# Optimization experiments

Measured on AMD Instinct MI355X. Metric: run time of the kernel, lower is better.

The kernel has to match this reference:

```python
import jax, jax.numpy as jnp
import numpy as np

N_HEAD = 16
D_MODEL = 1024
HEAD_DIM = D_MODEL // N_HEAD
B, S = 2, 2048


def setup_inputs() -> dict:
    key = jax.random.key(0)
    ks = jax.random.split(key, 7)
    qry = jax.random.normal(ks[0], (B, S, D_MODEL), dtype=jnp.float32)
    k_in = jax.random.normal(ks[1], (B, S, D_MODEL), dtype=jnp.float32)
    v_in = jax.random.normal(ks[2], (B, S, D_MODEL), dtype=jnp.float32)
    # causal boolean mask (B, S_q, S_k) as asserted in SelfAttention.forward
    attn_mask = jnp.broadcast_to(jnp.tril(jnp.ones((S, S), dtype=bool)), (B, S, S))
    scale = 1.0 / np.sqrt(D_MODEL)
    Wq = jax.random.normal(ks[3], (D_MODEL, D_MODEL), dtype=jnp.float32) * scale
    Wk = jax.random.normal(ks[4], (D_MODEL, D_MODEL), dtype=jnp.float32) * scale
    Wv = jax.random.normal(ks[5], (D_MODEL, D_MODEL), dtype=jnp.float32) * scale
    Wo = jax.random.normal(ks[6], (D_MODEL, D_MODEL), dtype=jnp.float32) * scale
    return {"qry": qry, "key": k_in, "val": v_in, "attn_mask": attn_mask,
            "Wq": Wq, "Wk": Wk, "Wv": Wv, "Wo": Wo}


def reference(qry, key, val, attn_mask, Wq, Wk, Wv, Wo):
    Bq, Sq, _ = qry.shape
    # torch Linear: y = x @ W.T (no bias)
    q = (qry @ Wq.T).reshape(Bq, Sq, N_HEAD, HEAD_DIM).transpose(0, 2, 1, 3)
    k = (key @ Wk.T).reshape(Bq, -1, N_HEAD, HEAD_DIM).transpose(0, 2, 1, 3)
    v = (val @ Wv.T).reshape(Bq, -1, N_HEAD, HEAD_DIM).transpose(0, 2, 1, 3)
    # scores: [B, H, Sq, Sk]
    scores = jnp.einsum('bhqd,bhkd->bhqk', q, k) / jnp.sqrt(jnp.float32(HEAD_DIM * N_HEAD) / N_HEAD)
    # attn_bias: 0 where mask True, -inf where False; broadcast over heads
    bias = jnp.where(attn_mask[:, None, :, :], 0.0, -jnp.inf).astype(scores.dtype)
    attn_weights = jax.nn.softmax(scores + bias, axis=-1)
    attn_feats = jnp.einsum('bhqk,bhkd->bhqd', attn_weights, v)
    attn_feats = attn_feats.transpose(0, 2, 1, 3).reshape(Bq, Sq, D_MODEL)
    output = attn_feats @ Wo.T
    return output, attn_weights
```

## Files before the change

kernel.cpp:

```cpp
#include <hip/hip_runtime.h>
#include <hip/hip_bf16.h>
#include <cstdint>
#include <cstddef>

#define DM 1024
#define NH 16
#define HD 64
#define BB 2
#define SS 2048

typedef __attribute__((ext_vector_type(4))) float f32x4;
typedef __attribute__((ext_vector_type(8))) short bf16x8;

typedef __attribute__((address_space(1))) const void GV;
typedef __attribute__((address_space(3))) void LV;

__global__ __launch_bounds__(256) void cvt_all(
    const float* s0, const float* s1, const float* s2, const float* s3,
    const float* s4, const float* s5, const float* s6,
    __hip_bfloat16* d0, __hip_bfloat16* d1, __hip_bfloat16* d2, __hip_bfloat16* d3,
    __hip_bfloat16* d4, __hip_bfloat16* d5, __hip_bfloat16* d6) {
    const float* s; __hip_bfloat16* d; int n4;
    switch (blockIdx.y) {
        case 0: s = s0; d = d0; n4 = 1 << 20; break;
        case 1: s = s1; d = d1; n4 = 1 << 20; break;
        case 2: s = s2; d = d2; n4 = 1 << 20; break;
        case 3: s = s3; d = d3; n4 = 1 << 18; break;
        case 4: s = s4; d = d4; n4 = 1 << 18; break;
        case 5: s = s5; d = d5; n4 = 1 << 18; break;
        default: s = s6; d = d6; n4 = 1 << 18; break;
    }
    for (int i = blockIdx.x * 256 + threadIdx.x; i < n4; i += 1024 * 256) {
        float4 v = reinterpret_cast<const float4*>(s)[i];
        ushort4 o;
        o.x = __builtin_bit_cast(unsigned short, __float2bfloat16(v.x));
        o.y = __builtin_bit_cast(unsigned short, __float2bfloat16(v.y));
        o.z = __builtin_bit_cast(unsigned short, __float2bfloat16(v.z));
        o.w = __builtin_bit_cast(unsigned short, __float2bfloat16(v.w));
        reinterpret_cast<ushort4*>(d)[i] = o;
    }
}

template <typename OutT>
__device__ __forceinline__ void gemm_body(const __hip_bfloat16* __restrict__ A,
                                          const __hip_bfloat16* __restrict__ Bw,
                                          OutT* __restrict__ C, int M, int N, int K,
                                          float alpha,
                                          __hip_bfloat16* As, __hip_bfloat16* Bs) {
    const int lane = threadIdx.x & 63;
    const int wv = threadIdx.x >> 6;
    const int wr = wv >> 1, wc = wv & 1;
    const int g = lane >> 4, cq = lane & 15;
    const int tM = blockIdx.y * 128, tN = blockIdx.x * 128;

    f32x4 acc[4][4];
#pragma unroll
    for (int i = 0; i < 4; ++i)
#pragma unroll
        for (int j = 0; j < 4; ++j) acc[i][j] = (f32x4){0.f, 0.f, 0.f, 0.f};

    for (int k0 = 0; k0 < K; k0 += 32) {
        __syncthreads();
#pragma unroll
        for (int r = 0; r < 2; ++r) {
            int chunk = r * 256 + wv * 64 + lane;
            int row = chunk >> 2;
            int kk = (chunk & 3) * 8;
            __builtin_amdgcn_global_load_lds((GV*)(A + (size_t)(tM + row) * K + k0 + kk),
                                             (LV*)(As + (size_t)(r * 256 + wv * 64) * 8), 16, 0, 0);
            __builtin_amdgcn_global_load_lds((GV*)(Bw + (size_t)(tN + row) * K + k0 + kk),
                                             (LV*)(Bs + (size_t)(r * 256 + wv * 64) * 8), 16, 0, 0);
        }
        __syncthreads();

        bf16x8 af[4], bfr[4];
#pragma unroll
        for (int i = 0; i < 4; ++i)
            af[i] = *reinterpret_cast<const bf16x8*>(As + (wr * 64 + i * 16 + cq) * 32 + g * 8);
#pragma unroll
        for (int j = 0; j < 4; ++j)
            bfr[j] = *reinterpret_cast<const bf16x8*>(Bs + (wc * 64 + j * 16 + cq) * 32 + g * 8);
#pragma unroll
        for (int i = 0; i < 4; ++i)
#pragma unroll
            for (int j = 0; j < 4; ++j)
                acc[i][j] = __builtin_amdgcn_mfma_f32_16x16x32_bf16(af[i], bfr[j], acc[i][j], 0, 0, 0);
    }

#pragma unroll
    for (int i = 0; i < 4; ++i)
#pragma unroll
        for (int j = 0; j < 4; ++j)
#pragma unroll
            for (int rr = 0; rr < 4; ++rr) {
                int row = tM + wr * 64 + i * 16 + g * 4 + rr;
                int col = tN + wc * 64 + j * 16 + cq;
                float v = acc[i][j][rr] * alpha;
                if constexpr (__is_same(OutT, float)) {
                    C[(size_t)row * N + col] = v;
                } else {
                    C[(size_t)row * N + col] = __float2bfloat16(v);
                }
            }
}

#define QALPHA 0.1803368801111204f

__global__ __launch_bounds__(256) void gemm_qkv(
    const __hip_bfloat16* qa, const __hip_bfloat16* ka, const __hip_bfloat16* va,
    const __hip_bfloat16* wq, const __hip_bfloat16* wk, const __hip_bfloat16* wv,
    __hip_bfloat16* Qm, __hip_bfloat16* Km, __hip_bfloat16* Vm) {
    __shared__ __hip_bfloat16 As[128 * 32];
    __shared__ __hip_bfloat16 Bs[128 * 32];
    const __hip_bfloat16 *A, *Bw;
    __hip_bfloat16* C;
    float alpha = 1.0f;
    switch (blockIdx.z) {
        case 0: A = qa; Bw = wq; C = Qm; alpha = QALPHA; break;
        case 1: A = ka; Bw = wk; C = Km; break;
        default: A = va; Bw = wv; C = Vm; break;
    }
    gemm_body<__hip_bfloat16>(A, Bw, C, BB * SS, DM, DM, alpha, As, Bs);
}

__global__ __launch_bounds__(256) void gemm_out(const __hip_bfloat16* __restrict__ A,
                                                const __hip_bfloat16* __restrict__ Bw,
                                                float* __restrict__ C) {
    __shared__ __hip_bfloat16 As[128 * 32];
    __shared__ __hip_bfloat16 Bs[128 * 32];
    gemm_body<float>(A, Bw, C, BB * SS, DM, DM, 1.0f, As, Bs);
}

__global__ __launch_bounds__(256) void transpose_v(const __hip_bfloat16* __restrict__ V,
                                                   __hip_bfloat16* __restrict__ VT) {
    const int bh = blockIdx.x;
    const int b = bh >> 4, h = bh & 15;
    const int k0 = blockIdx.y * 64;
    __shared__ __hip_bfloat16 tile[64][68];
    const int r = threadIdx.x >> 4;
    const int c4 = threadIdx.x & 15;
#pragma unroll
    for (int rr = r; rr < 64; rr += 16) {
        ushort4 u = *reinterpret_cast<const ushort4*>(
            V + (size_t)(b * SS + k0 + rr) * DM + h * HD + c4 * 4);
        *reinterpret_cast<ushort4*>(&tile[rr][c4 * 4]) = u;
    }
    __syncthreads();
#pragma unroll
    for (int dd = r; dd < 64; dd += 16) {
        ushort4 o;
        o.x = __builtin_bit_cast(unsigned short, tile[c4 * 4 + 0][dd]);
        o.y = __builtin_bit_cast(unsigned short, tile[c4 * 4 + 1][dd]);
        o.z = __builtin_bit_cast(unsigned short, tile[c4 * 4 + 2][dd]);
        o.w = __builtin_bit_cast(unsigned short, tile[c4 * 4 + 3][dd]);
        *reinterpret_cast<ushort4*>(VT + ((size_t)bh * HD + dd) * SS + k0 + c4 * 4) = o;
    }
}

__global__ __launch_bounds__(256) void attn_fused(const __hip_bfloat16* __restrict__ Q,
                                                  const __hip_bfloat16* __restrict__ Kb,
                                                  const __hip_bfloat16* __restrict__ VT,
                                                  float* __restrict__ Wout,
                                                  __hip_bfloat16* __restrict__ feats) {
    __shared__ __hip_bfloat16 klds[2][64][64];
    __shared__ __hip_bfloat16 vlds[2][64][64];
    __shared__ __hip_bfloat16 plds[4][16][64];
    const int qt = (SS / 64 - 1) - blockIdx.x;
    const int bh = blockIdx.y;
    const int b = bh >> 4, h = bh & 15;
    const int lane = threadIdx.x & 63;
    const int wv = threadIdx.x >> 6;
    const int g = lane >> 4, cq = lane & 15;
    const int q0w = qt * 64 + wv * 16;
    const size_t rowbase = (size_t)b * SS;
    const int tmaxw = q0w >> 4;

    const __hip_bfloat16* qp = Q + (rowbase + q0w + cq) * DM + h * HD + g * 8;
    const bf16x8 qf0 = *reinterpret_cast<const bf16x8*>(qp);
    const bf16x8 qf1 = *reinterpret_cast<const bf16x8*>(qp + 32);

    auto stageK = [&](int kc, int buf) {
#pragma unroll
        for (int i = 0; i < 2; ++i) {
            int slot = i * 256 + wv * 64 + lane;
            int row = slot >> 3, c16 = slot & 7;
            const __hip_bfloat16* src =
                Kb + (rowbase + kc * 64 + row) * DM + h * HD + ((c16 ^ (row & 7)) << 3);
            __builtin_amdgcn_global_load_lds(
                (GV*)src, (LV*)(&klds[buf][0][0] + (size_t)(i * 256 + wv * 64) * 8), 16, 0, 0);
        }
    };
    auto stageV = [&](int kc, int buf) {
#pragma unroll
        for (int i = 0; i < 2; ++i) {
            int slot = i * 256 + wv * 64 + lane;
            int row = slot >> 3, c16 = slot & 7;
            const __hip_bfloat16* src =
                VT + ((size_t)bh * HD + row) * SS + kc * 64 + ((c16 ^ (row & 7)) << 3);
            __builtin_amdgcn_global_load_lds(
                (GV*)src, (LV*)(&vlds[buf][0][0] + (size_t)(i * 256 + wv * 64) * 8), 16, 0, 0);
        }
    };

    const int swx = cq & 7;

    float l_[4] = {0.f, 0.f, 0.f, 0.f};
    stageK(0, 0);
    for (int kc = 0; kc <= qt; ++kc) {
        const int cur = kc & 1;
        __syncthreads();
        if (kc < qt) stageK(kc + 1, cur ^ 1);
#pragma unroll
        for (int hh = 0; hh < 4; ++hh) {
            const int kt = kc * 4 + hh;
            if (kt > tmaxw) break;
            const __hip_bfloat16* kb = &klds[cur][hh * 16 + cq][0];
            bf16x8 kf0 = *reinterpret_cast<const bf16x8*>(kb + ((g ^ swx) << 3));
            bf16x8 kf1 = *reinterpret_cast<const bf16x8*>(kb + (((4 + g) ^ swx) << 3));
            f32x4 sc = (f32x4){0.f, 0.f, 0.f, 0.f};
            sc = __builtin_amdgcn_mfma_f32_16x16x32_bf16(qf0, kf0, sc, 0, 0, 0);
            sc = __builtin_amdgcn_mfma_f32_16x16x32_bf16(qf1, kf1, sc, 0, 0, 0);
            const int kk = kt * 16 + cq;
#pragma unroll
            for (int r = 0; r < 4; ++r) {
                const int qr = q0w + g * 4 + r;
                float p = (kk <= qr) ? __builtin_amdgcn_exp2f(sc[r]) : 0.0f;
                l_[r] += p;
            }
        }
    }
    float invl[4];
#pragma unroll
    for (int r = 0; r < 4; ++r) {
        float l = l_[r];
#pragma unroll
        for (int mk = 1; mk < 16; mk <<= 1) l += __shfl_xor(l, mk);
        invl[r] = __builtin_amdgcn_rcpf(l);
    }

    f32x4 oacc[4];
#pragma unroll
    for (int j = 0; j < 4; ++j) oacc[j] = (f32x4){0.f, 0.f, 0.f, 0.f};

    __syncthreads();
    stageK(0, 0);
    stageV(0, 0);
    for (int kc = 0; kc <= qt; ++kc) {
        const int cur = kc & 1;
        __syncthreads();
        if (kc < qt) { stageK(kc + 1, cur ^ 1); stageV(kc + 1, cur ^ 1); }

#pragma unroll
        for (int hh = 0; hh < 4; ++hh) {
            const int kt = kc * 4 + hh;
            if (kt <= tmaxw) {
                const __hip_bfloat16* kb = &klds[cur][hh * 16 + cq][0];
                bf16x8 kf0 = *reinterpret_cast<const bf16x8*>(kb + ((g ^ swx) << 3));
                bf16x8 kf1 = *reinterpret_cast<const bf16x8*>(kb + (((4 + g) ^ swx) << 3));
                f32x4 sc = (f32x4){0.f, 0.f, 0.f, 0.f};
                sc = __builtin_amdgcn_mfma_f32_16x16x32_bf16(qf0, kf0, sc, 0, 0, 0);
                sc = __builtin_amdgcn_mfma_f32_16x16x32_bf16(qf1, kf1, sc, 0, 0, 0);
                const int kk = kt * 16 + cq;
#pragma unroll
                for (int r = 0; r < 4; ++r) {
                    const int row = g * 4 + r;
                    const int qr = q0w + row;
                    float w = (kk <= qr) ? __builtin_amdgcn_exp2f(sc[r]) * invl[r] : 0.0f;
                    plds[wv][row][(hh * 16 + cq) ^ (8 * (row & 7))] = __float2bfloat16(w);
                }
            } else {
#pragma unroll
                for (int r = 0; r < 4; ++r) {
                    const int row = g * 4 + r;
                    plds[wv][row][(hh * 16 + cq) ^ (8 * (row & 7))] = __float2bfloat16(0.0f);
                }
            }
        }

        const int sw = 8 * swx;
        bf16x8 wa0 = *reinterpret_cast<const bf16x8*>(&plds[wv][cq][(g * 8) ^ sw]);
        bf16x8 wa1 = *reinterpret_cast<const bf16x8*>(&plds[wv][cq][(32 + g * 8) ^ sw]);
        __builtin_amdgcn_s_setprio(1);
#pragma unroll
        for (int j = 0; j < 4; ++j) {
            const __hip_bfloat16* vb = &vlds[cur][j * 16 + cq][0];
            bf16x8 vb0 = *reinterpret_cast<const bf16x8*>(vb + ((g ^ swx) << 3));
            bf16x8 vb1 = *reinterpret_cast<const bf16x8*>(vb + (((4 + g) ^ swx) << 3));
            oacc[j] = __builtin_amdgcn_mfma_f32_16x16x32_bf16(wa0, vb0, oacc[j], 0, 0, 0);
            oacc[j] = __builtin_amdgcn_mfma_f32_16x16x32_bf16(wa1, vb1, oacc[j], 0, 0, 0);
        }
        __builtin_amdgcn_s_setprio(0);

#pragma unroll
        for (int rh = 0; rh < 2; ++rh)
#pragma unroll
            for (int ch = 0; ch < 2; ++ch) {
                const int row = rh * 8 + (lane >> 3);
                const int fc = ch * 32 + (lane & 7) * 4;
                ushort4 u = *reinterpret_cast<const ushort4*>(
                    &plds[wv][row][fc ^ (8 * (row & 7))]);
                f32x4 v4;
                v4[0] = __builtin_bit_cast(float, (uint32_t)u.x << 16);
                v4[1] = __builtin_bit_cast(float, (uint32_t)u.y << 16);
                v4[2] = __builtin_bit_cast(float, (uint32_t)u.z << 16);
                v4[3] = __builtin_bit_cast(float, (uint32_t)u.w << 16);
                __builtin_nontemporal_store(
                    v4, reinterpret_cast<f32x4*>(
                            Wout + ((size_t)bh * SS + q0w + row) * SS + kc * 64 + fc));
            }
    }

    const int zstart = (qt + 1) * 64;
    const f32x4 z4 = (f32x4){0.f, 0.f, 0.f, 0.f};
    const int zrow = lane >> 2;
    const int zc = (lane & 3) * 4;
    for (int c = zstart; c < SS; c += 64) {
#pragma unroll
        for (int it = 0; it < 4; ++it) {
            f32x4* p = reinterpret_cast<f32x4*>(
                Wout + ((size_t)bh * SS + q0w + zrow) * SS + c + it * 16 + zc);
            __builtin_nontemporal_store(z4, p);
        }
    }

#pragma unroll
    for (int j = 0; j < 4; ++j)
#pragma unroll
        for (int r = 0; r < 4; ++r)
            feats[(rowbase + q0w + g * 4 + r) * DM + h * HD + j * 16 + cq] =
                __float2bfloat16(oacc[j][r]);
}

extern "C" void kernel_launch(void* const* d_in, const int* in_sizes, int n_in,
                              void* d_out, int out_size, void* d_ws, size_t ws_size,
                              hipStream_t stream) {
    (void)in_sizes; (void)n_in; (void)out_size;
    const float* qry = (const float*)d_in[0];
    const float* key = (const float*)d_in[1];
    const float* val = (const float*)d_in[2];
    const float* Wq = (const float*)d_in[4];
    const float* Wk = (const float*)d_in[5];
    const float* Wv = (const float*)d_in[6];
    const float* Wo = (const float*)d_in[7];

    float* out = (float*)d_out;
    float* w_out = out + (size_t)BB * SS * DM;

    const size_t E = (size_t)BB * SS * DM;
    const size_t W = (size_t)DM * DM;
    if (ws_size < (8 * E + 4 * W) * sizeof(__hip_bfloat16)) return;

    __hip_bfloat16* ws = (__hip_bfloat16*)d_ws;
    __hip_bfloat16* qb    = ws;
    __hip_bfloat16* kb    = ws + E;
    __hip_bfloat16* vb    = ws + 2 * E;
    __hip_bfloat16* wqb   = ws + 3 * E;
    __hip_bfloat16* wkb   = ws + 3 * E + W;
    __hip_bfloat16* wvb   = ws + 3 * E + 2 * W;
    __hip_bfloat16* wob   = ws + 3 * E + 3 * W;
    __hip_bfloat16* Qm    = ws + 3 * E + 4 * W;
    __hip_bfloat16* Km    = ws + 4 * E + 4 * W;
    __hip_bfloat16* Vm    = ws + 5 * E + 4 * W;
    __hip_bfloat16* VTm   = ws + 6 * E + 4 * W;
    __hip_bfloat16* feats = ws + 7 * E + 4 * W;

    cvt_all<<<dim3(1024, 7), 256, 0, stream>>>(qry, key, val, Wq, Wk, Wv, Wo,
                                               qb, kb, vb, wqb, wkb, wvb, wob);

    gemm_qkv<<<dim3(DM / 128, (BB * SS) / 128, 3), 256, 0, stream>>>(
        qb, kb, vb, wqb, wkb, wvb, Qm, Km, Vm);

    transpose_v<<<dim3(BB * NH, SS / 64), 256, 0, stream>>>(Vm, VTm);

    attn_fused<<<dim3(SS / 64, BB * NH), 256, 0, stream>>>(Qm, Km, VTm, w_out, feats);

    gemm_out<<<dim3(DM / 128, (BB * SS) / 128), 256, 0, stream>>>(feats, wob, out);
}
```

Before: 282.8 us.

## Deepen K prefetch pipeline with explicit vmcnt waits and raw barriers

Replaces the separate K and V double buffers with one pool of four LDS tiles. The first (row-sum) pass now prefetches K three tiles ahead, and the second pass issues the next K and V tiles at the top of each iteration. `__syncthreads` is replaced by explicit `s_waitcnt vmcnt` plus `s_barrier` at the end of each iteration, so earlier loads stay in flight rather than being drained at every barrier. The vmcnt thresholds depend on the exact count of outstanding memory ops, including the nontemporal Wout stores. Tail iterations also issue redundant loads of the last tile.

```diff
diff --git a/kernel.cpp b/kernel.cpp
--- a/kernel.cpp
+++ b/kernel.cpp
@@ -14,6 +14,9 @@
 
 typedef __attribute__((address_space(1))) const void GV;
 typedef __attribute__((address_space(3))) void LV;
+
+#define WAITV(N) asm volatile("s_waitcnt vmcnt(" N ")" ::: "memory")
+#define SBAR do { __builtin_amdgcn_s_barrier(); asm volatile("" ::: "memory"); } while (0)
 
 __global__ __launch_bounds__(256) void cvt_all(
     const float* s0, const float* s1, const float* s2, const float* s3,
@@ -162,8 +165,7 @@
                                                   const __hip_bfloat16* __restrict__ VT,
                                                   float* __restrict__ Wout,
                                                   __hip_bfloat16* __restrict__ feats) {
-    __shared__ __hip_bfloat16 klds[2][64][64];
-    __shared__ __hip_bfloat16 vlds[2][64][64];
+    __shared__ __hip_bfloat16 sbuf[4][64 * 64];
     __shared__ __hip_bfloat16 plds[4][16][64];
     const int qt = (SS / 64 - 1) - blockIdx.x;
     const int bh = blockIdx.y;
@@ -179,7 +181,7 @@
     const bf16x8 qf0 = *reinterpret_cast<const bf16x8*>(qp);
     const bf16x8 qf1 = *reinterpret_cast<const bf16x8*>(qp + 32);
 
-    auto stageK = [&](int kc, int buf) {
+    auto stageK = [&](int kc, __hip_bfloat16* dst) {
 #pragma unroll
         for (int i = 0; i < 2; ++i) {
             int slot = i * 256 + wv * 64 + lane;
@@ -187,10 +189,10 @@
             const __hip_bfloat16* src =
                 Kb + (rowbase + kc * 64 + row) * DM + h * HD + ((c16 ^ (row & 7)) << 3);
             __builtin_amdgcn_global_load_lds(
-                (GV*)src, (LV*)(&klds[buf][0][0] + (size_t)(i * 256 + wv * 64) * 8), 16, 0, 0);
+                (GV*)src, (LV*)(dst + (size_t)(i * 256 + wv * 64) * 8), 16, 0, 0);
         }
     };
-    auto stageV = [&](int kc, int buf) {
+    auto stageV = [&](int kc, __hip_bfloat16* dst) {
 #pragma unroll
         for (int i = 0; i < 2; ++i) {
             int slot = i * 256 + wv * 64 + lane;
@@ -198,23 +200,27 @@
             const __hip_bfloat16* src =
                 VT + ((size_t)bh * HD + row) * SS + kc * 64 + ((c16 ^ (row & 7)) << 3);
             __builtin_amdgcn_global_load_lds(
-                (GV*)src, (LV*)(&vlds[buf][0][0] + (size_t)(i * 256 + wv * 64) * 8), 16, 0, 0);
+                (GV*)src, (LV*)(dst + (size_t)(i * 256 + wv * 64) * 8), 16, 0, 0);
         }
     };
 
     const int swx = cq & 7;
 
     float l_[4] = {0.f, 0.f, 0.f, 0.f};
-    stageK(0, 0);
+    stageK(0, sbuf[0]);
+    stageK(qt < 1 ? qt : 1, sbuf[1]);
+    stageK(qt < 2 ? qt : 2, sbuf[2]);
+    WAITV("4");
+    SBAR;
     for (int kc = 0; kc <= qt; ++kc) {
-        const int cur = kc & 1;
-        __syncthreads();
-        if (kc < qt) stageK(kc + 1, cur ^ 1);
+        const int nx = kc + 3;
+        stageK(nx > qt ? qt : nx, sbuf[nx & 3]);
+        const __hip_bfloat16* kbase = sbuf[kc & 3];
 #pragma unroll
         for (int hh = 0; hh < 4; ++hh) {
             const int kt = kc * 4 + hh;
             if (kt > tmaxw) break;
-            const __hip_bfloat16* kb = &klds[cur][hh * 16 + cq][0];
+            const __hip_bfloat16* kb = kbase + (hh * 16 + cq) * 64;
             bf16x8 kf0 = *reinterpret_cast<const bf16x8*>(kb + ((g ^ swx) << 3));
             bf16x8 kf1 = *reinterpret_cast<const bf16x8*>(kb + (((4 + g) ^ swx) << 3));
             f32x4 sc = (f32x4){0.f, 0.f, 0.f, 0.f};
@@ -224,9 +230,12 @@
 #pragma unroll
             for (int r = 0; r < 4; ++r) {
                 const int qr = q0w + g * 4 + r;
-                float p = (kk <= qr) ? __builtin_amdgcn_exp2f(sc[r]) : 0.0f;
-                l_[r] += p;
+                l_[r] += (kk <= qr) ? __builtin_amdgcn_exp2f(sc[r]) : 0.0f;
             }
+        }
+        if (kc < qt) {
+            WAITV("4");
+            SBAR;
         }
     }
     float invl[4];
@@ -242,19 +251,24 @@
 #pragma unroll
     for (int j = 0; j < 4; ++j) oacc[j] = (f32x4){0.f, 0.f, 0.f, 0.f};
 
-    __syncthreads();
-    stageK(0, 0);
-    stageV(0, 0);
+    SBAR;
+    stageK(0, sbuf[0]);
+    stageV(0, sbuf[2]);
+    WAITV("0");
+    SBAR;
     for (int kc = 0; kc <= qt; ++kc) {
-        const int cur = kc & 1;
-        __syncthreads();
-        if (kc < qt) { stageK(kc + 1, cur ^ 1); stageV(kc + 1, cur ^ 1); }
+        const int nx = kc + 1;
+        const int nc = nx > qt ? qt : nx;
+        stageK(nc, sbuf[nx & 1]);
+        stageV(nc, sbuf[2 + (nx & 1)]);
+        const __hip_bfloat16* kbase = sbuf[kc & 1];
+        const __hip_bfloat16* vbase = sbuf[2 + (kc & 1)];
 
 #pragma unroll
         for (int hh = 0; hh < 4; ++hh) {
             const int kt = kc * 4 + hh;
             if (kt <= tmaxw) {
-                const __hip_bfloat16* kb = &klds[cur][hh * 16 + cq][0];
+                const __hip_bfloat16* kb = kbase + (hh * 16 + cq) * 64;
                 bf16x8 kf0 = *reinterpret_cast<const bf16x8*>(kb + ((g ^ swx) << 3));
                 bf16x8 kf1 = *reinterpret_cast<const bf16x8*>(kb + (((4 + g) ^ swx) << 3));
                 f32x4 sc = (f32x4){0.f, 0.f, 0.f, 0.f};
@@ -283,7 +297,7 @@
         __builtin_amdgcn_s_setprio(1);
 #pragma unroll
         for (int j = 0; j < 4; ++j) {
-            const __hip_bfloat16* vb = &vlds[cur][j * 16 + cq][0];
+            const __hip_bfloat16* vb = vbase + (j * 16 + cq) * 64;
             bf16x8 vb0 = *reinterpret_cast<const bf16x8*>(vb + ((g ^ swx) << 3));
             bf16x8 vb1 = *reinterpret_cast<const bf16x8*>(vb + (((4 + g) ^ swx) << 3));
             oacc[j] = __builtin_amdgcn_mfma_f32_16x16x32_bf16(wa0, vb0, oacc[j], 0, 0, 0);
@@ -308,6 +322,11 @@
                     v4, reinterpret_cast<f32x4*>(
                             Wout + ((size_t)bh * SS + q0w + row) * SS + kc * 64 + fc));
             }
+
+        if (kc < qt) {
+            WAITV("4");
+            SBAR;
+        }
     }
 
     const int zstart = (qt + 1) * 64;
```

Measured after the change: 278.9 us. About the same (-1.4%).
